# Optimization experiments

Measured on AMD Instinct MI355X. Metric: run time of the kernel, lower is better.

Reference implementation:

```python
import jax, jax.numpy as jnp
import numpy as np

B, N, C, R, E = 8, 4096, 128, 16, 65536


def setup_inputs() -> dict:
    key = jax.random.key(0)
    ks = jax.random.split(key, 8)
    node_features = jax.random.normal(ks[0], (B, N, C), dtype=jnp.float32)
    edge_index = jax.random.randint(ks[1], (B, 2, E), 0, N, dtype=jnp.int64)
    edge_type = jax.random.randint(ks[2], (B, E), 0, R, dtype=jnp.int64)
    s = 1.0 / np.sqrt(C)
    rel_weight = jax.random.uniform(ks[3], (R, C, C), jnp.float32, -s, s)
    root_weight = jax.random.uniform(ks[4], (C, C), jnp.float32, -s, s)
    rgcn_bias = jnp.zeros((C,), jnp.float32)
    lin_weight = jax.random.uniform(ks[5], (C, 1), jnp.float32, -s, s)
    lin_bias = jnp.zeros((1,), jnp.float32)
    return {
        'node_features': node_features,
        'edge_index': edge_index,
        'edge_type': edge_type,
        'rel_weight': rel_weight,
        'root_weight': root_weight,
        'rgcn_bias': rgcn_bias,
        'lin_weight': lin_weight,
        'lin_bias': lin_bias,
    }


def _rgcn_score(node_features, edge_index, edge_type, rel_weight, root_weight,
                rgcn_bias, lin_weight, lin_bias):
    # Flatten batch of graphs into one big disjoint graph (as batch_rgcn does).
    x = node_features.reshape(B * N, C)
    offs = (jnp.arange(B, dtype=edge_index.dtype) * N)[:, None, None]  # (B,1,1)
    ei = (edge_index + offs).transpose(1, 0, 2).reshape(2, B * E)  # (2, B*E)
    et = edge_type.reshape(B * E)
    src, dst = ei[0], ei[1]

    x_src = x[src]  # (B*E, C) gathered source features
    # root transform + bias (RGCNConv root_weight + bias)
    out = x @ root_weight + rgcn_bias  # (B*N, C)
    # per-relation mean aggregation; mean(W_r x_j) == W_r mean(x_j)
    for r in range(R):
        mask = (et == r).astype(x.dtype)  # (B*E,)
        s = jax.ops.segment_sum(x_src * mask[:, None], dst, num_segments=B * N)
        cnt = jax.ops.segment_sum(mask, dst, num_segments=B * N)
        mean = jnp.where(cnt[:, None] > 0, s / jnp.maximum(cnt, 1.0)[:, None], 0.0)
        out = out + mean @ rel_weight[r]

    out = jax.nn.relu(out)  # dropout is identity at eval
    scores = (out @ lin_weight + lin_bias).reshape(B, N)
    return scores


def reference(node_features, edge_index, edge_type, rel_weight, root_weight,
              rgcn_bias, lin_weight, lin_bias):
    return _rgcn_score(node_features, edge_index, edge_type, rel_weight,
                       root_weight, rgcn_bias, lin_weight, lin_bias)
```

## Files before the change

kernel.cpp:

```cpp
#include <hip/hip_runtime.h>

#define BB 8
#define NN 4096
#define CC 128
#define RR 16
#define EE 65536
#define NNODES 32768
#define NEDGES 524288
#define KTOT   2176
#define LDP    80
#define CSP    136
#define BCAP   60
#define GEMMB  4352

typedef unsigned short ushort_t;
typedef short bf16x8 __attribute__((ext_vector_type(8)));
typedef float f32x4 __attribute__((ext_vector_type(4)));

__device__ __forceinline__ unsigned short f2b(float f) {
    unsigned u = __builtin_bit_cast(unsigned, f);
    unsigned r = (u + 0x7fffu + ((u >> 16) & 1u)) >> 16;
    return (unsigned short)r;
}
__device__ __forceinline__ float b2f(unsigned short s) {
    return __builtin_bit_cast(float, (unsigned)s << 16);
}
__device__ __forceinline__ float ldf(const void* p, int j, int isbf) {
    return isbf ? b2f(((const ushort_t*)p)[j]) : ((const float*)p)[j];
}
__device__ __forceinline__ int ldi(const int* p, int j, int is64) {
    return p[j << is64];
}

__device__ __forceinline__ int probe_isbf(const ushort_t* xf) {
    int t = threadIdx.x & 63;
    int bad = 0;
    for (int j = t; j < 512; j += 64) {
        unsigned e = (xf[j] >> 7) & 0xffu;
        if (e >= 160u) bad = 1;
    }
    return __ballot(bad) == 0ull;
}

__global__ __launch_bounds__(256) void prep_k(const void* __restrict__ x,
                                              const void* __restrict__ relw,
                                              const void* __restrict__ rootw,
                                              const int* __restrict__ ei,
                                              const int* __restrict__ et,
                                              ushort_t* __restrict__ Xb,
                                              ushort_t* __restrict__ WT,
                                              int* __restrict__ dcnt,
                                              int* __restrict__ flags) {
    int bx = blockIdx.x, t = threadIdx.x;
    if (bx < 2048) {
        int isbf = probe_isbf((const ushort_t*)x);
        int tid = bx * 256 + t;
        if (isbf) {
            ((uint4*)Xb)[tid] = ((const uint4*)x)[tid];
        } else {
            const float4* xf = (const float4*)x;
            float4 a = xf[2 * tid], b = xf[2 * tid + 1];
            ushort4 o0, o1;
            o0.x = f2b(a.x); o0.y = f2b(a.y); o0.z = f2b(a.z); o0.w = f2b(a.w);
            o1.x = f2b(b.x); o1.y = f2b(b.y); o1.z = f2b(b.z); o1.w = f2b(b.w);
            ((ushort4*)Xb)[2 * tid] = o0; ((ushort4*)Xb)[2 * tid + 1] = o1;
        }
    } else if (bx < 3136) {
        int isbf = probe_isbf((const ushort_t*)x);
        int tid = (bx - 2048) * 256 + t;
        int nglob = tid >> 7, k = tid & 127;
        int jb = nglob >> 7, n = nglob & 127;
        float v = (jb == 0) ? ldf(rootw, k * 128 + n, isbf)
                            : ldf(relw, ((jb - 1) << 14) + k * 128 + n, isbf);
        WT[tid] = f2b(v);
    } else if (bx < 3168) {
        int tid = (bx - 3136) * 256 + t;
        ((uint4*)dcnt)[tid] = make_uint4(0, 0, 0, 0);
    } else {
        if (t < 64) {
            int isbf = probe_isbf((const ushort_t*)x);
            int a = (t < 16) ? ei[2 * t + 1] : 0;
            int b = (t < 16) ? et[2 * t + 1] : 0;
            unsigned long long ma = __ballot(a != 0);
            unsigned long long mb = __ballot(b != 0);
            if (t == 0) {
                flags[0] = isbf;
                flags[1] = (ma == 0ull);
                flags[2] = (mb == 0ull);
            }
        }
    }
}

__global__ __launch_bounds__(256) void ge_k(const ushort_t* __restrict__ Xb,
                                            const ushort_t* __restrict__ WT,
                                            ushort_t* __restrict__ Y,
                                            const int* __restrict__ ei,
                                            const int* __restrict__ et,
                                            int* __restrict__ dcnt,
                                            int* __restrict__ bucket,
                                            const int* __restrict__ flags) {
    __shared__ ushort_t smem[2 * 128 * LDP];
    int bx = blockIdx.x, t = threadIdx.x;
    if (bx >= GEMMB) {
        int w64i = flags[1], w64t = flags[2];
        int tid = (bx - GEMMB) * 256 + t;
        int b = tid >> 16, e = tid & 65535;
        int src = ldi(ei, (b * 2) * EE + e, w64i);
        int dst = ldi(ei, (b * 2 + 1) * EE + e, w64i);
        int r = ldi(et, tid, w64t);
        int gd = (b << 12) + dst;
        int pos = atomicAdd(&dcnt[gd], 1);
        if (pos < BCAP)
            bucket[gd * BCAP + pos] = (((b << 12) + src) << 4) | r;
        return;
    }
    ushort_t* As = smem;
    ushort_t* Bs = smem + 128 * LDP;
    int m0 = (bx & 255) * 128, n0 = (bx >> 8) * 128;
    int wave = t >> 6, lane = t & 63, lrow = lane & 15, lq = lane >> 4;
    int wm = (wave >> 1) * 64, wn = (wave & 1) * 64;
    f32x4 acc[4][4] = {};

    for (int kt = 0; kt < 2; ++kt) {
        #pragma unroll
        for (int i = 0; i < 4; ++i) {
            int c = t + i * 256;
            int row = c >> 3, c8 = c & 7;
            uint4 va = *(const uint4*)(Xb + (size_t)(m0 + row) * 128 + kt * 64 + c8 * 8);
            *(uint4*)(&As[row * LDP + c8 * 8]) = va;
            uint4 vb = *(const uint4*)(WT + (size_t)(n0 + row) * 128 + kt * 64 + c8 * 8);
            *(uint4*)(&Bs[row * LDP + c8 * 8]) = vb;
        }
        __syncthreads();
        #pragma unroll
        for (int ks = 0; ks < 2; ++ks) {
            int k0 = ks * 32 + lq * 8;
            bf16x8 a[4], b[4];
            #pragma unroll
            for (int mi = 0; mi < 4; ++mi) a[mi] = *(const bf16x8*)(&As[(wm + mi * 16 + lrow) * LDP + k0]);
            #pragma unroll
            for (int ni = 0; ni < 4; ++ni) b[ni] = *(const bf16x8*)(&Bs[(wn + ni * 16 + lrow) * LDP + k0]);
            #pragma unroll
            for (int mi = 0; mi < 4; ++mi)
                #pragma unroll
                for (int ni = 0; ni < 4; ++ni)
                    acc[mi][ni] = __builtin_amdgcn_mfma_f32_16x16x32_bf16(a[mi], b[ni], acc[mi][ni], 0, 0, 0);
        }
        __syncthreads();
    }
    ushort_t* Cs = smem;
    #pragma unroll
    for (int mi = 0; mi < 4; ++mi)
        #pragma unroll
        for (int rg = 0; rg < 4; ++rg) {
            int row = wm + mi * 16 + lq * 4 + rg;
            #pragma unroll
            for (int ni = 0; ni < 4; ++ni)
                Cs[row * CSP + wn + ni * 16 + lrow] = f2b(acc[mi][ni][rg]);
        }
    __syncthreads();
    #pragma unroll
    for (int i = 0; i < 8; ++i) {
        int c = t + i * 256;
        int row = c >> 4, c16 = c & 15;
        uint4 v = *(const uint4*)(&Cs[row * CSP + c16 * 8]);
        *(uint4*)(Y + (size_t)(m0 + row) * KTOT + n0 + c16 * 8) = v;
    }
}

__global__ __launch_bounds__(128) void agg_score_k(const ushort_t* __restrict__ Y,
                                                   const int* __restrict__ dcnt,
                                                   const int* __restrict__ bucket,
                                                   const void* __restrict__ bias,
                                                   const void* __restrict__ linw,
                                                   const void* __restrict__ linb,
                                                   void* __restrict__ out,
                                                   const int* __restrict__ flags) {
    int i = blockIdx.x, t = threadIdx.x;
    int isbf = flags[0];
    __shared__ int scnt[RR];
    __shared__ float inv[RR];
    int nc = dcnt[i]; if (nc > BCAP) nc = BCAP;
    const int* bk = bucket + i * BCAP;
    if (t < RR) scnt[t] = 0;
    __syncthreads();
    if (t < nc) atomicAdd(&scnt[bk[t] & 15], 1);
    __syncthreads();
    if (t < RR) inv[t] = (scnt[t] > 0) ? 1.0f / (float)scnt[t] : 0.0f;
    __syncthreads();

    float acc = b2f(Y[(size_t)i * KTOT + t]) + ldf(bias, t, isbf);
    int e = 0;
    for (; e + 7 < nc; e += 8) {
        int v[8]; float y[8];
        #pragma unroll
        for (int j = 0; j < 8; ++j) v[j] = bk[e + j];
        #pragma unroll
        for (int j = 0; j < 8; ++j)
            y[j] = b2f(Y[(size_t)(v[j] >> 4) * KTOT + CC + ((v[j] & 15) << 7) + t]);
        #pragma unroll
        for (int j = 0; j < 8; ++j) acc += inv[v[j] & 15] * y[j];
    }
    for (; e + 3 < nc; e += 4) {
        int v0 = bk[e], v1 = bk[e + 1], v2 = bk[e + 2], v3 = bk[e + 3];
        float y0 = b2f(Y[(size_t)(v0 >> 4) * KTOT + CC + ((v0 & 15) << 7) + t]);
        float y1 = b2f(Y[(size_t)(v1 >> 4) * KTOT + CC + ((v1 & 15) << 7) + t]);
        float y2 = b2f(Y[(size_t)(v2 >> 4) * KTOT + CC + ((v2 & 15) << 7) + t]);
        float y3 = b2f(Y[(size_t)(v3 >> 4) * KTOT + CC + ((v3 & 15) << 7) + t]);
        acc += inv[v0 & 15] * y0 + inv[v1 & 15] * y1 + inv[v2 & 15] * y2 + inv[v3 & 15] * y3;
    }
    for (; e < nc; ++e) {
        int v = bk[e];
        acc += inv[v & 15] * b2f(Y[(size_t)(v >> 4) * KTOT + CC + ((v & 15) << 7) + t]);
    }
    float val = fmaxf(acc, 0.f) * ldf(linw, t, isbf);
    for (int o = 32; o > 0; o >>= 1) val += __shfl_down(val, o, 64);
    __shared__ float red[2];
    if ((t & 63) == 0) red[t >> 6] = val;
    __syncthreads();
    if (t == 0) {
        float res = red[0] + red[1] + ldf(linb, 0, isbf);
        if (isbf) ((ushort_t*)out)[i] = f2b(res);
        else      ((float*)out)[i] = res;
    }
}

extern "C" void kernel_launch(void* const* d_in, const int* in_sizes, int n_in,
                              void* d_out, int out_size, void* d_ws, size_t ws_size,
                              hipStream_t stream) {
    const void* x     = d_in[0];
    const int*  ei    = (const int*)d_in[1];
    const int*  et    = (const int*)d_in[2];
    const void* relw  = d_in[3];
    const void* rootw = d_in[4];
    const void* bias  = d_in[5];
    const void* linw  = d_in[6];
    const void* linb  = d_in[7];

    const size_t WS_NEED = 159547904;
    if (ws_size < WS_NEED) return;

    char* ws = (char*)d_ws;
    ushort_t* Y      = (ushort_t*)(ws);
    ushort_t* Xb     = (ushort_t*)(ws + 142606336);
    ushort_t* WT     = (ushort_t*)(ws + 150994944);
    int*      dcnt   = (int*)(ws + 151552000);
    int*      bucket = (int*)(ws + 151683072);
    int*      flags  = (int*)(ws + 159547392);

    prep_k<<<3169, 256, 0, stream>>>(x, relw, rootw, ei, et, Xb, WT, dcnt, flags);
    ge_k<<<GEMMB + 2048, 256, 0, stream>>>(Xb, WT, Y, ei, et, dcnt, bucket, flags);
    agg_score_k<<<NNODES, 128, 0, stream>>>(Y, dcnt, bucket, bias, linw, linb, d_out, flags);
}
```

Before: 178.2 us.

## Vectorize edge gathers in aggregation and schedule edge-bucketing blocks first

The aggregation kernel now splits its 128 threads into 8 groups of 16. Each group loads a full 128-channel bf16 row with 16-byte vector loads, one edge per group, and the partial sums are reduced through shared memory. This replaces the scalar 2-byte-per-thread gathers. The fused GEMM/bucketing kernel also places the edge-bucketing blocks at the front of the grid, so they are dispatched first and can overlap with the GEMM blocks. The cost is extra shared memory and a barrier for the partial-sum reduction.

```diff
diff --git a/kernel.cpp b/kernel.cpp
--- a/kernel.cpp
+++ b/kernel.cpp
@@ -12,6 +12,7 @@
 #define CSP    136
 #define BCAP   60
 #define GEMMB  4352
+#define EDGEB  2048
 
 typedef unsigned short ushort_t;
 typedef short bf16x8 __attribute__((ext_vector_type(8)));
@@ -102,9 +103,9 @@
                                             const int* __restrict__ flags) {
     __shared__ ushort_t smem[2 * 128 * LDP];
     int bx = blockIdx.x, t = threadIdx.x;
-    if (bx >= GEMMB) {
+    if (bx < EDGEB) {
         int w64i = flags[1], w64t = flags[2];
-        int tid = (bx - GEMMB) * 256 + t;
+        int tid = bx * 256 + t;
         int b = tid >> 16, e = tid & 65535;
         int src = ldi(ei, (b * 2) * EE + e, w64i);
         int dst = ldi(ei, (b * 2 + 1) * EE + e, w64i);
@@ -115,9 +116,10 @@
             bucket[gd * BCAP + pos] = (((b << 12) + src) << 4) | r;
         return;
     }
+    int bxg = bx - EDGEB;
     ushort_t* As = smem;
     ushort_t* Bs = smem + 128 * LDP;
-    int m0 = (bx & 255) * 128, n0 = (bx >> 8) * 128;
+    int m0 = (bxg & 255) * 128, n0 = (bxg >> 8) * 128;
     int wave = t >> 6, lane = t & 63, lrow = lane & 15, lq = lane >> 4;
     int wm = (wave >> 1) * 64, wn = (wave & 1) * 64;
     f32x4 acc[4][4] = {};
@@ -181,39 +183,43 @@
     int isbf = flags[0];
     __shared__ int scnt[RR];
     __shared__ float inv[RR];
+    __shared__ int bke[64];
+    __shared__ float part[128][9];
     int nc = dcnt[i]; if (nc > BCAP) nc = BCAP;
     const int* bk = bucket + i * BCAP;
     if (t < RR) scnt[t] = 0;
     __syncthreads();
-    if (t < nc) atomicAdd(&scnt[bk[t] & 15], 1);
+    if (t < nc) { int v = bk[t]; bke[t] = v; atomicAdd(&scnt[v & 15], 1); }
     __syncthreads();
     if (t < RR) inv[t] = (scnt[t] > 0) ? 1.0f / (float)scnt[t] : 0.0f;
     __syncthreads();
 
+    int g = t >> 4, l16 = t & 15;
+    float a8[8] = {};
+    for (int base = 0; base < nc; base += 8) {
+        int e = base + g;
+        if (e < nc) {
+            int v = bke[e];
+            const ushort_t* yr = Y + (size_t)(v >> 4) * KTOT + CC + ((v & 15) << 7) + l16 * 8;
+            uint4 u = *(const uint4*)yr;
+            float w = inv[v & 15];
+            a8[0] += w * __builtin_bit_cast(float, u.x << 16);
+            a8[1] += w * __builtin_bit_cast(float, u.x & 0xffff0000u);
+            a8[2] += w * __builtin_bit_cast(float, u.y << 16);
+            a8[3] += w * __builtin_bit_cast(float, u.y & 0xffff0000u);
+            a8[4] += w * __builtin_bit_cast(float, u.z << 16);
+            a8[5] += w * __builtin_bit_cast(float, u.z & 0xffff0000u);
+            a8[6] += w * __builtin_bit_cast(float, u.w << 16);
+            a8[7] += w * __builtin_bit_cast(float, u.w & 0xffff0000u);
+        }
+    }
+    #pragma unroll
+    for (int j = 0; j < 8; ++j) part[l16 * 8 + j][g] = a8[j];
+    __syncthreads();
+
     float acc = b2f(Y[(size_t)i * KTOT + t]) + ldf(bias, t, isbf);
-    int e = 0;
-    for (; e + 7 < nc; e += 8) {
-        int v[8]; float y[8];
-        #pragma unroll
-        for (int j = 0; j < 8; ++j) v[j] = bk[e + j];
-        #pragma unroll
-        for (int j = 0; j < 8; ++j)
-            y[j] = b2f(Y[(size_t)(v[j] >> 4) * KTOT + CC + ((v[j] & 15) << 7) + t]);
-        #pragma unroll
-        for (int j = 0; j < 8; ++j) acc += inv[v[j] & 15] * y[j];
-    }
-    for (; e + 3 < nc; e += 4) {
-        int v0 = bk[e], v1 = bk[e + 1], v2 = bk[e + 2], v3 = bk[e + 3];
-        float y0 = b2f(Y[(size_t)(v0 >> 4) * KTOT + CC + ((v0 & 15) << 7) + t]);
-        float y1 = b2f(Y[(size_t)(v1 >> 4) * KTOT + CC + ((v1 & 15) << 7) + t]);
-        float y2 = b2f(Y[(size_t)(v2 >> 4) * KTOT + CC + ((v2 & 15) << 7) + t]);
-        float y3 = b2f(Y[(size_t)(v3 >> 4) * KTOT + CC + ((v3 & 15) << 7) + t]);
-        acc += inv[v0 & 15] * y0 + inv[v1 & 15] * y1 + inv[v2 & 15] * y2 + inv[v3 & 15] * y3;
-    }
-    for (; e < nc; ++e) {
-        int v = bk[e];
-        acc += inv[v & 15] * b2f(Y[(size_t)(v >> 4) * KTOT + CC + ((v & 15) << 7) + t]);
-    }
+    #pragma unroll
+    for (int gg = 0; gg < 8; ++gg) acc += part[t][gg];
     float val = fmaxf(acc, 0.f) * ldf(linw, t, isbf);
     for (int o = 32; o > 0; o >>= 1) val += __shfl_down(val, o, 64);
     __shared__ float red[2];
@@ -250,6 +256,6 @@
     int*      flags  = (int*)(ws + 159547392);
 
     prep_k<<<3169, 256, 0, stream>>>(x, relw, rootw, ei, et, Xb, WT, dcnt, flags);
-    ge_k<<<GEMMB + 2048, 256, 0, stream>>>(Xb, WT, Y, ei, et, dcnt, bucket, flags);
+    ge_k<<<EDGEB + GEMMB, 256, 0, stream>>>(Xb, WT, Y, ei, et, dcnt, bucket, flags);
     agg_score_k<<<NNODES, 128, 0, stream>>>(Y, dcnt, bucket, bias, linw, linb, d_out, flags);
 }
```

New measurement: 167.0 us, median of 2. -6.3%, faster.
